# Kernel optimization log

Measured on AMD Instinct MI355X. Metric: run time of the kernel, lower is better.

The kernel has to match this reference:

```python
import jax, jax.numpy as jnp
import numpy as np
from jax.scipy.special import logsumexp

NEG = -1e9  # stands in for log(0) = -inf in the padded one-hots (avoids NaN-producing -inf)


def setup_inputs() -> dict:
    key = jax.random.key(0)
    ks = jax.random.split(key, 9)
    Lx, Ly, B, D, Vout = 64, 64, 128, 256, 53
    return {
        "prior_ctx": jax.random.normal(ks[0], (Lx, B, D), dtype=jnp.float32),
        "modern_ctx": jax.random.normal(ks[1], (Ly, B, D), dtype=jnp.float32),
        "W_sub": jax.random.normal(ks[2], (Vout, D), dtype=jnp.float32) * 0.05,
        "b_sub": jax.random.normal(ks[3], (Vout,), dtype=jnp.float32) * 0.05,
        "W_ins": jax.random.normal(ks[4], (Vout, D), dtype=jnp.float32) * 0.05,
        "b_ins": jax.random.normal(ks[5], (Vout,), dtype=jnp.float32) * 0.05,
        "target_ids": jax.random.randint(ks[6], (Ly - 1, B), 0, Vout, dtype=jnp.int32),
        "src_lengths": jax.random.randint(ks[7], (B,), 1, Lx + 1),
        "tgt_lengths": jax.random.randint(ks[8], (B,), 1, Ly + 1),
    }


def reference(prior_ctx, modern_ctx, W_sub, b_sub, W_ins, b_ins,
              target_ids, src_lengths, tgt_lengths):
    Lx, B, D = prior_ctx.shape
    Ly = modern_ctx.shape[0]
    Vout = W_sub.shape[0]

    # outer-sum context: [Lx, Ly, B, D]
    ctx = prior_ctx[:, None, :, :] + modern_ctx[None, :, :, :]

    # padding matrix: True where both source pos i and target pos j are valid. [Lx, Ly, B, 1]
    mask = ((jnp.arange(Lx)[:, None, None] < src_lengths[None, None, :])
            & (jnp.arange(Ly)[None, :, None] < tgt_lengths[None, None, :]))[..., None]

    # heads: Linear + LogSoftmax, zeroed on padding. [Lx, Ly, B, Vout]
    sub = jnp.where(mask, jax.nn.log_softmax(jnp.einsum('xybd,vd->xybv', ctx, W_sub) + b_sub, axis=-1), 0.0)
    ins = jnp.where(mask, jax.nn.log_softmax(jnp.einsum('xybd,vd->xybv', ctx, W_ins) + b_ins, axis=-1), 0.0)

    del_probs = sub[:, :, :, Vout - 1]  # [Lx, Ly, B]
    end_probs = ins[:, :, :, Vout - 1]

    # log one-hots of targets shifted by 1: [Ly-1, B, Vout]
    log_oh = jnp.where(target_ids[:, :, None] == jnp.arange(Vout)[None, None, :], 0.0, NEG)

    sub_probs = logsumexp(sub[:, :-1] + log_oh[None], axis=-1)  # [Lx, Ly-1, B]
    ins_probs = logsumexp(ins[:, :-1] + log_oh[None], axis=-1)
    return del_probs, end_probs, sub_probs, ins_probs
```

## Files before the change

kernel.cpp:

```cpp
#include <hip/hip_runtime.h>

#define D   256
#define NB  128
#define NV  53
#define NR  8192
#define V4  14
#define SLB (V4*NR*4)


typedef float  f4 __attribute__((ext_vector_type(4)));
typedef short  s8 __attribute__((ext_vector_type(8)));

__device__ __forceinline__ ushort f2bf(float f) {
    uint u = __float_as_uint(f);
    u += 0x7fff + ((u >> 16) & 1);
    return (ushort)(u >> 16);
}
__device__ __forceinline__ float bflo(uint w) { return __uint_as_float(w << 16); }
__device__ __forceinline__ float bfhi(uint w) { return __uint_as_float(w & 0xffff0000u); }

__global__ __launch_bounds__(256) void p1_kernel(
    const float* __restrict__ prior, const float* __restrict__ modern,
    const float* __restrict__ Wsub, const float* __restrict__ bsub,
    const float* __restrict__ Wins, const float* __restrict__ bins,
    ushort* __restrict__ wsb)
{
    __shared__ ushort WB[3584 * 8];
    const int tid = threadIdx.x;

    #pragma unroll
    for (int i = 0; i < 14; ++i) {
        const int F  = tid + 256 * i;
        const int l  = F & 63, s = (F >> 6) & 7, nt = F >> 9;
        const int o  = nt * 16 + (l & 15);
        const int d0 = 32 * s + 8 * (l >> 4);
        s8 bfr;
        if (o < NV) {
            const float* w = Wsub + o * D + d0;
            #pragma unroll
            for (int j = 0; j < 8; ++j) bfr[j] = (short)f2bf(w[j]);
        } else if (o < 106) {
            const float* w = Wins + (o - NV) * D + d0;
            #pragma unroll
            for (int j = 0; j < 8; ++j) bfr[j] = (short)f2bf(w[j]);
        } else {
            #pragma unroll
            for (int j = 0; j < 8; ++j) bfr[j] = 0;
        }
        *(s8*)&WB[F * 8] = bfr;
    }
    __syncthreads();

    const int wave = tid >> 6, lane = tid & 63;
    const int tile = blockIdx.x * 4 + wave;
    const int side = tile >> 9;
    const int row0 = (tile & 511) << 4;
    const int lrow = lane & 15, lk = lane >> 4;
    const float* __restrict__ src =
        (side ? modern : prior) + (size_t)(row0 + lrow) * D + lk * 8;

    f4 acc[7];
    #pragma unroll
    for (int nt = 0; nt < 7; ++nt) { acc[nt][0]=0.f; acc[nt][1]=0.f; acc[nt][2]=0.f; acc[nt][3]=0.f; }

    #pragma unroll
    for (int s = 0; s < 8; ++s) {
        const f4 c0 = *(const f4*)(src + 32 * s);
        const f4 c1 = *(const f4*)(src + 32 * s + 4);
        s8 a;
        a[0]=(short)f2bf(c0[0]); a[1]=(short)f2bf(c0[1]);
        a[2]=(short)f2bf(c0[2]); a[3]=(short)f2bf(c0[3]);
        a[4]=(short)f2bf(c1[0]); a[5]=(short)f2bf(c1[1]);
        a[6]=(short)f2bf(c1[2]); a[7]=(short)f2bf(c1[3]);
        #pragma unroll
        for (int nt = 0; nt < 7; ++nt) {
            const s8 bfr = *(const s8*)&WB[(((nt << 3) + s) * 64 + lane) * 8];
            acc[nt] = __builtin_amdgcn_mfma_f32_16x16x32_bf16(a, bfr, acc[nt], 0, 0, 0);
        }
    }

    ushort* __restrict__ base = wsb + side * (2 * SLB);
    #pragma unroll
    for (int nt = 0; nt < 7; ++nt) {
        const int v = nt * 16 + lrow;
        if (v < 106) {
            float bias = 0.f;
            if (side) bias = (v < NV) ? bsub[v] : bins[v - NV];
            const int   vi = (v < NV) ? v : v - NV;
            ushort* sl     = base + ((v < NV) ? 0 : SLB);
            const int a0   = (vi >> 2) * (NR * 4) + (vi & 3);
            #pragma unroll
            for (int r = 0; r < 4; ++r) {
                const int row = row0 + 4 * lk + r;
                sl[a0 + row * 4] = f2bf(acc[nt][r] + bias);
            }
        }
    }
}

__global__ __launch_bounds__(256) void p2_kernel(
    const ushort* __restrict__ wsb,
    const int* __restrict__ target, const int* __restrict__ srclen,
    const int* __restrict__ tgtlen, float* __restrict__ out)
{
    const int tid = threadIdx.x;
    const int b   = tid & 127;
    const int bid = blockIdx.x;
    const int xt  = ((bid & 7) << 1) | ((bid >> 3) & 1);
    const int y   = ((bid >> 4) << 1) | (tid >> 7);
    const int yb  = y * NB + b;

    const int sl = srclen[b], tl = tgtlen[b];
    const bool ymask = y < tl;
    const bool hasT  = y < 63;
    const int  t     = hasT ? target[y * NB + b] : 0;
    const int  toff  = (t >> 2) * (NR * 4) + (t & 3);

    float m[56], l[56];

    #pragma unroll
    for (int dist = 0; dist < 2; ++dist) {
        const ushort* __restrict__ P = wsb + dist * SLB;
        const ushort* __restrict__ M = wsb + (2 + dist) * SLB;

        #pragma unroll
        for (int g = 0; g < V4; ++g) {
            const uint2 q = *(const uint2*)(M + (g * NR + yb) * 4);
            m[4*g+0] = bflo(q.x); m[4*g+1] = bfhi(q.x);
            m[4*g+2] = bflo(q.y); m[4*g+3] = bfhi(q.y);
        }
        const float mlt = bflo((uint)M[toff + yb * 4]);

        float* __restrict__ o0 = out + dist * 524288;
        float* __restrict__ o1 = out + 1048576 + dist * 516096;

        #pragma unroll
        for (int xi = 0; xi < 4; ++xi) {
            const int x  = (xt << 2) + xi;
            const int xb = x * NB + b;
            const bool msk = (x < sl) & ymask;
            #pragma unroll
            for (int g = 0; g < V4; ++g) {
                const uint2 q = *(const uint2*)(P + (g * NR + xb) * 4);
                l[4*g+0] = bflo(q.x) + m[4*g+0];
                l[4*g+1] = bfhi(q.x) + m[4*g+1];
                l[4*g+2] = bflo(q.y) + m[4*g+2];
                l[4*g+3] = bfhi(q.y) + m[4*g+3];
            }
            float mx = l[0];
            #pragma unroll
            for (int v = 1; v < NV; ++v) mx = fmaxf(mx, l[v]);
            float ssum = 0.f;
            #pragma unroll
            for (int v = 0; v < NV; ++v) ssum += __expf(l[v] - mx);
            const float lse = mx + __logf(ssum);
            o0[((x << 6) | y) * NB + b] = msk ? (l[NV - 1] - lse) : 0.f;
            if (hasT) {
                const float lt = bflo((uint)P[toff + xb * 4]) + mlt;
                o1[(x * 63 + y) * NB + b] = msk ? (lt - lse) : 0.f;
            }
        }
    }
}

extern "C" void kernel_launch(void* const* d_in, const int* in_sizes, int n_in,
                              void* d_out, int out_size, void* d_ws, size_t ws_size,
                              hipStream_t stream) {
    const float* prior  = (const float*)d_in[0];
    const float* modern = (const float*)d_in[1];
    const float* Wsub   = (const float*)d_in[2];
    const float* bsub   = (const float*)d_in[3];
    const float* Wins   = (const float*)d_in[4];
    const float* bins   = (const float*)d_in[5];
    const int*   target = (const int*)d_in[6];
    const int*   srclen = (const int*)d_in[7];
    const int*   tgtlen = (const int*)d_in[8];
    ushort* wsb = (ushort*)d_ws;
    float*  out = (float*)d_out;

    p1_kernel<<<256, 256, 0, stream>>>(prior, modern, Wsub, bsub, Wins, bins, wsb);
    p2_kernel<<<512, 256, 0, stream>>>(wsb, target, srclen, tgtlen, out);
}
```

Measured before the change: 36.01 us.

## Pre-pack weights once, subtract per-row maxima, drop max pass from logsumexp

```diff
diff --git a/kernel.cpp b/kernel.cpp
--- a/kernel.cpp
+++ b/kernel.cpp
@@ -6,9 +6,14 @@
 #define NR  8192
 #define V4  14
 #define SLB (V4*NR*4)
+#define WBOFF (4*SLB)
+#define BTOFF (WBOFF + 3584*8)
+#define LOG2E 1.44269504088896340736f
+#define LN2   0.69314718055994530942f
 
 
 typedef float  f4 __attribute__((ext_vector_type(4)));
+typedef float  f2 __attribute__((ext_vector_type(2)));
 typedef short  s8 __attribute__((ext_vector_type(8)));
 
 __device__ __forceinline__ ushort f2bf(float f) {
@@ -19,38 +24,57 @@
 __device__ __forceinline__ float bflo(uint w) { return __uint_as_float(w << 16); }
 __device__ __forceinline__ float bfhi(uint w) { return __uint_as_float(w & 0xffff0000u); }
 
-__global__ __launch_bounds__(256) void p1_kernel(
+__device__ __forceinline__ float fexp2(float x) {
+#if __has_builtin(__builtin_amdgcn_exp2f)
+    return __builtin_amdgcn_exp2f(x);
+#else
+    return exp2f(x);
+#endif
+}
+__device__ __forceinline__ float flog2(float x) {
+#if __has_builtin(__builtin_amdgcn_logf)
+    return __builtin_amdgcn_logf(x);
+#else
+    return log2f(x);
+#endif
+}
+
+__global__ void p0_kernel(const float* __restrict__ Wsub, const float* __restrict__ Wins,
+                          const float* __restrict__ bsub, const float* __restrict__ bins,
+                          ushort* __restrict__ WBg, float* __restrict__ biasT)
+{
+    const int F  = blockIdx.x * 64 + threadIdx.x;
+    const int l  = F & 63, s = (F >> 6) & 7, nt = F >> 9;
+    const int o  = nt * 16 + (l & 15);
+    const int d0 = 32 * s + 8 * (l >> 4);
+    s8 bfr;
+    if (o < NV) {
+        const float* w = Wsub + o * D + d0;
+        #pragma unroll
+        for (int j = 0; j < 8; ++j) bfr[j] = (short)f2bf(w[j] * LOG2E);
+    } else if (o < 106) {
+        const float* w = Wins + (o - NV) * D + d0;
+        #pragma unroll
+        for (int j = 0; j < 8; ++j) bfr[j] = (short)f2bf(w[j] * LOG2E);
+    } else {
+        #pragma unroll
+        for (int j = 0; j < 8; ++j) bfr[j] = 0;
+    }
+    *(s8*)&WBg[F * 8] = bfr;
+    if (F < 112) {
+        float bv = 0.f;
+        if (F < NV)       bv = bsub[F] * LOG2E;
+        else if (F < 106) bv = bins[F - NV] * LOG2E;
+        biasT[F] = bv;
+    }
+}
+
+__global__ __launch_bounds__(256, 1) void p1_kernel(
     const float* __restrict__ prior, const float* __restrict__ modern,
-    const float* __restrict__ Wsub, const float* __restrict__ bsub,
-    const float* __restrict__ Wins, const float* __restrict__ bins,
+    const ushort* __restrict__ WBg, const float* __restrict__ biasT,
     ushort* __restrict__ wsb)
 {
-    __shared__ ushort WB[3584 * 8];
-    const int tid = threadIdx.x;
-
-    #pragma unroll
-    for (int i = 0; i < 14; ++i) {
-        const int F  = tid + 256 * i;
-        const int l  = F & 63, s = (F >> 6) & 7, nt = F >> 9;
-        const int o  = nt * 16 + (l & 15);
-        const int d0 = 32 * s + 8 * (l >> 4);
-        s8 bfr;
-        if (o < NV) {
-            const float* w = Wsub + o * D + d0;
-            #pragma unroll
-            for (int j = 0; j < 8; ++j) bfr[j] = (short)f2bf(w[j]);
-        } else if (o < 106) {
-            const float* w = Wins + (o - NV) * D + d0;
-            #pragma unroll
-            for (int j = 0; j < 8; ++j) bfr[j] = (short)f2bf(w[j]);
-        } else {
-            #pragma unroll
-            for (int j = 0; j < 8; ++j) bfr[j] = 0;
-        }
-        *(s8*)&WB[F * 8] = bfr;
-    }
-    __syncthreads();
-
+    const int tid  = threadIdx.x;
     const int wave = tid >> 6, lane = tid & 63;
     const int tile = blockIdx.x * 4 + wave;
     const int side = tile >> 9;
@@ -74,8 +98,40 @@
         a[6]=(short)f2bf(c1[2]); a[7]=(short)f2bf(c1[3]);
         #pragma unroll
         for (int nt = 0; nt < 7; ++nt) {
-            const s8 bfr = *(const s8*)&WB[(((nt << 3) + s) * 64 + lane) * 8];
+            const s8 bfr = *(const s8*)&WBg[(((nt << 3) + s) * 64 + lane) * 8];
             acc[nt] = __builtin_amdgcn_mfma_f32_16x16x32_bf16(a, bfr, acc[nt], 0, 0, 0);
+        }
+    }
+
+    float val[7][4];
+    #pragma unroll
+    for (int nt = 0; nt < 7; ++nt) {
+        const int v = nt * 16 + lrow;
+        const float bias = side ? biasT[v] : 0.f;
+        #pragma unroll
+        for (int r = 0; r < 4; ++r) val[nt][r] = acc[nt][r] + bias;
+    }
+
+    float ms[4], mi[4];
+    #pragma unroll
+    for (int r = 0; r < 4; ++r) { ms[r] = -3e38f; mi[r] = -3e38f; }
+    #pragma unroll
+    for (int nt = 0; nt < 7; ++nt) {
+        const int v = nt * 16 + lrow;
+        const bool isS = v < NV;
+        const bool isI = (v >= NV) & (v < 106);
+        #pragma unroll
+        for (int r = 0; r < 4; ++r) {
+            ms[r] = fmaxf(ms[r], isS ? val[nt][r] : -3e38f);
+            mi[r] = fmaxf(mi[r], isI ? val[nt][r] : -3e38f);
+        }
+    }
+    #pragma unroll
+    for (int r = 0; r < 4; ++r) {
+        #pragma unroll
+        for (int k = 1; k <= 8; k <<= 1) {
+            ms[r] = fmaxf(ms[r], __shfl_xor(ms[r], k));
+            mi[r] = fmaxf(mi[r], __shfl_xor(mi[r], k));
         }
     }
 
@@ -84,21 +140,35 @@
     for (int nt = 0; nt < 7; ++nt) {
         const int v = nt * 16 + lrow;
         if (v < 106) {
-            float bias = 0.f;
-            if (side) bias = (v < NV) ? bsub[v] : bins[v - NV];
-            const int   vi = (v < NV) ? v : v - NV;
-            ushort* sl     = base + ((v < NV) ? 0 : SLB);
+            const bool isS = v < NV;
+            const int  vi  = isS ? v : v - NV;
+            ushort* sl     = base + (isS ? 0 : SLB);
             const int a0   = (vi >> 2) * (NR * 4) + (vi & 3);
             #pragma unroll
             for (int r = 0; r < 4; ++r) {
                 const int row = row0 + 4 * lk + r;
-                sl[a0 + row * 4] = f2bf(acc[nt][r] + bias);
-            }
-        }
-    }
-}
-
-__global__ __launch_bounds__(256) void p2_kernel(
+                const float rm = isS ? ms[r] : mi[r];
+                sl[a0 + row * 4] = f2bf(val[nt][r] - rm);
+            }
+        }
+    }
+    {
+        const int v6 = 96 + lrow;
+        if (v6 >= 106 && v6 <= 108) {
+            const int vi = v6 - NV;
+            const int a0 = (vi >> 2) * (NR * 4) + (vi & 3);
+            const ushort PADBF = f2bf(-1e30f);
+            #pragma unroll
+            for (int r = 0; r < 4; ++r) {
+                const int row = row0 + 4 * lk + r;
+                base[a0 + row * 4]       = PADBF;
+                base[SLB + a0 + row * 4] = PADBF;
+            }
+        }
+    }
+}
+
+__global__ __launch_bounds__(256, 2) void p2_kernel(
     const ushort* __restrict__ wsb,
     const int* __restrict__ target, const int* __restrict__ srclen,
     const int* __restrict__ tgtlen, float* __restrict__ out)
@@ -116,18 +186,17 @@
     const int  t     = hasT ? target[y * NB + b] : 0;
     const int  toff  = (t >> 2) * (NR * 4) + (t & 3);
 
-    float m[56], l[56];
-
     #pragma unroll
     for (int dist = 0; dist < 2; ++dist) {
         const ushort* __restrict__ P = wsb + dist * SLB;
         const ushort* __restrict__ M = wsb + (2 + dist) * SLB;
 
+        f2 Ml[V4], Mh[V4];
         #pragma unroll
         for (int g = 0; g < V4; ++g) {
             const uint2 q = *(const uint2*)(M + (g * NR + yb) * 4);
-            m[4*g+0] = bflo(q.x); m[4*g+1] = bfhi(q.x);
-            m[4*g+2] = bflo(q.y); m[4*g+3] = bfhi(q.y);
+            Ml[g][0] = bflo(q.x); Ml[g][1] = bfhi(q.x);
+            Mh[g][0] = bflo(q.y); Mh[g][1] = bfhi(q.y);
         }
         const float mlt = bflo((uint)M[toff + yb * 4]);
 
@@ -139,25 +208,29 @@
             const int x  = (xt << 2) + xi;
             const int xb = x * NB + b;
             const bool msk = (x < sl) & ymask;
+
+            f2 sa; sa[0] = 0.f; sa[1] = 0.f;
+            f2 sb; sb[0] = 0.f; sb[1] = 0.f;
+            float l52 = 0.f;
             #pragma unroll
             for (int g = 0; g < V4; ++g) {
-                const uint2 q = *(const uint2*)(P + (g * NR + xb) * 4);
-                l[4*g+0] = bflo(q.x) + m[4*g+0];
-                l[4*g+1] = bfhi(q.x) + m[4*g+1];
-                l[4*g+2] = bflo(q.y) + m[4*g+2];
-                l[4*g+3] = bfhi(q.y) + m[4*g+3];
-            }
-            float mx = l[0];
-            #pragma unroll
-            for (int v = 1; v < NV; ++v) mx = fmaxf(mx, l[v]);
-            float ssum = 0.f;
-            #pragma unroll
-            for (int v = 0; v < NV; ++v) ssum += __expf(l[v] - mx);
-            const float lse = mx + __logf(ssum);
-            o0[((x << 6) | y) * NB + b] = msk ? (l[NV - 1] - lse) : 0.f;
+                const uint2 p = *(const uint2*)(P + (g * NR + xb) * 4);
+                f2 av; av[0] = bflo(p.x); av[1] = bfhi(p.x);
+                f2 bv; bv[0] = bflo(p.y); bv[1] = bfhi(p.y);
+                av = av + Ml[g];
+                bv = bv + Mh[g];
+                if (g == 13) l52 = av[0];
+                f2 ea; ea[0] = fexp2(av[0]); ea[1] = fexp2(av[1]);
+                f2 eb; eb[0] = fexp2(bv[0]); eb[1] = fexp2(bv[1]);
+                sa = sa + ea;
+                sb = sb + eb;
+            }
+            const f2 st = sa + sb;
+            const float ls = flog2(st[0] + st[1]);
+            o0[((x << 6) | y) * NB + b] = msk ? (l52 - ls) * LN2 : 0.f;
             if (hasT) {
                 const float lt = bflo((uint)P[toff + xb * 4]) + mlt;
-                o1[(x * 63 + y) * NB + b] = msk ? (lt - lse) : 0.f;
+                o1[(x * 63 + y) * NB + b] = msk ? (lt - ls) * LN2 : 0.f;
             }
         }
     }
@@ -175,9 +248,12 @@
     const int*   target = (const int*)d_in[6];
     const int*   srclen = (const int*)d_in[7];
     const int*   tgtlen = (const int*)d_in[8];
-    ushort* wsb = (ushort*)d_ws;
-    float*  out = (float*)d_out;
-
-    p1_kernel<<<256, 256, 0, stream>>>(prior, modern, Wsub, bsub, Wins, bins, wsb);
+    ushort* wsb   = (ushort*)d_ws;
+    ushort* WBg   = wsb + WBOFF;
+    float*  biasT = (float*)(wsb + BTOFF);
+    float*  out   = (float*)d_out;
+
+    p0_kernel<<<56, 64, 0, stream>>>(Wsub, Wins, bsub, bins, WBg, biasT);
+    p1_kernel<<<256, 256, 0, stream>>>(prior, modern, WBg, biasT, wsb);
     p2_kernel<<<512, 256, 0, stream>>>(wsb, target, srclen, tgtlen, out);
 }
```

Result: slower. 41.80 us (+16.1%).

## Factorize softmax sum into products of precomputed exponentials and split weight prep

Applied to the files above, without the earlier changes.

```diff
diff --git a/kernel.cpp b/kernel.cpp
--- a/kernel.cpp
+++ b/kernel.cpp
@@ -6,9 +6,16 @@
 #define NR  8192
 #define V4  14
 #define SLB (V4*NR*4)
+#define ESOFF (4*SLB)
+#define WBOFF (8*SLB)
+#define BTOFF (WBOFF + 3584*8)
+#define A52   (13*NR*4)
+#define LOG2E 1.44269504088896340736f
+#define LN2   0.69314718055994530942f
 
 
 typedef float  f4 __attribute__((ext_vector_type(4)));
+typedef float  f2 __attribute__((ext_vector_type(2)));
 typedef short  s8 __attribute__((ext_vector_type(8)));
 
 __device__ __forceinline__ ushort f2bf(float f) {
@@ -18,50 +25,63 @@
 }
 __device__ __forceinline__ float bflo(uint w) { return __uint_as_float(w << 16); }
 __device__ __forceinline__ float bfhi(uint w) { return __uint_as_float(w & 0xffff0000u); }
-
-__global__ __launch_bounds__(256) void p1_kernel(
+__device__ __forceinline__ float fexp2(float x) { return __builtin_exp2f(x); }
+__device__ __forceinline__ float flog2(float x) { return __builtin_log2f(x); }
+
+__global__ void p0_kernel(const float* __restrict__ Wsub, const float* __restrict__ Wins,
+                          const float* __restrict__ bsub, const float* __restrict__ bins,
+                          ushort* __restrict__ WBg, float* __restrict__ biasT)
+{
+    const int F  = blockIdx.x * 64 + threadIdx.x;
+    const int l  = F & 63, s = (F >> 6) & 7, nt = F >> 9;
+    const int o  = nt * 16 + (l & 15);
+    const int d0 = 32 * s + 8 * (l >> 4);
+    s8 bfr;
+    if (o < NV) {
+        const float* w = Wsub + o * D + d0;
+        #pragma unroll
+        for (int j = 0; j < 8; ++j) bfr[j] = (short)f2bf(w[j] * LOG2E);
+    } else if (o < 106) {
+        const float* w = Wins + (o - NV) * D + d0;
+        #pragma unroll
+        for (int j = 0; j < 8; ++j) bfr[j] = (short)f2bf(w[j] * LOG2E);
+    } else {
+        #pragma unroll
+        for (int j = 0; j < 8; ++j) bfr[j] = 0;
+    }
+    *(s8*)&WBg[F * 8] = bfr;
+    if (F < 112) {
+        float bv = 0.f;
+        if (F < NV)       bv = bsub[F] * LOG2E;
+        else if (F < 106) bv = bins[F - NV] * LOG2E;
+        biasT[F] = bv;
+    }
+}
+
+template<int NT0, int NTN>
+__device__ __forceinline__ void p1_body(
     const float* __restrict__ prior, const float* __restrict__ modern,
-    const float* __restrict__ Wsub, const float* __restrict__ bsub,
-    const float* __restrict__ Wins, const float* __restrict__ bins,
-    ushort* __restrict__ wsb)
-{
-    __shared__ ushort WB[3584 * 8];
-    const int tid = threadIdx.x;
-
-    #pragma unroll
-    for (int i = 0; i < 14; ++i) {
-        const int F  = tid + 256 * i;
-        const int l  = F & 63, s = (F >> 6) & 7, nt = F >> 9;
-        const int o  = nt * 16 + (l & 15);
-        const int d0 = 32 * s + 8 * (l >> 4);
-        s8 bfr;
-        if (o < NV) {
-            const float* w = Wsub + o * D + d0;
-            #pragma unroll
-            for (int j = 0; j < 8; ++j) bfr[j] = (short)f2bf(w[j]);
-        } else if (o < 106) {
-            const float* w = Wins + (o - NV) * D + d0;
-            #pragma unroll
-            for (int j = 0; j < 8; ++j) bfr[j] = (short)f2bf(w[j]);
-        } else {
-            #pragma unroll
-            for (int j = 0; j < 8; ++j) bfr[j] = 0;
-        }
-        *(s8*)&WB[F * 8] = bfr;
+    const ushort* __restrict__ WBg, const float* __restrict__ biasT,
+    ushort* __restrict__ wsb, ushort* __restrict__ WB, int tid, int tg)
+{
+    #pragma unroll
+    for (int i = 0; i < NTN * 2; ++i) {
+        const int idx = i * 256 + tid;
+        *(s8*)&WB[idx * 8] = *(const s8*)&WBg[(NT0 * 512 + idx) * 8];
     }
     __syncthreads();
 
     const int wave = tid >> 6, lane = tid & 63;
-    const int tile = blockIdx.x * 4 + wave;
+    const int tile = tg * 4 + wave;
     const int side = tile >> 9;
     const int row0 = (tile & 511) << 4;
     const int lrow = lane & 15, lk = lane >> 4;
     const float* __restrict__ src =
         (side ? modern : prior) + (size_t)(row0 + lrow) * D + lk * 8;
 
-    f4 acc[7];
-    #pragma unroll
-    for (int nt = 0; nt < 7; ++nt) { acc[nt][0]=0.f; acc[nt][1]=0.f; acc[nt][2]=0.f; acc[nt][3]=0.f; }
+    f4 acc[NTN];
+    #pragma unroll
+    for (int j = 0; j < NTN; ++j) { acc[j][0]=0.f; acc[j][1]=0.f; acc[j][2]=0.f; acc[j][3]=0.f; }
 
     #pragma unroll
     for (int s = 0; s < 8; ++s) {
@@ -73,29 +93,58 @@
         a[4]=(short)f2bf(c1[0]); a[5]=(short)f2bf(c1[1]);
         a[6]=(short)f2bf(c1[2]); a[7]=(short)f2bf(c1[3]);
         #pragma unroll
-        for (int nt = 0; nt < 7; ++nt) {
-            const s8 bfr = *(const s8*)&WB[(((nt << 3) + s) * 64 + lane) * 8];
-            acc[nt] = __builtin_amdgcn_mfma_f32_16x16x32_bf16(a, bfr, acc[nt], 0, 0, 0);
-        }
-    }
-
-    ushort* __restrict__ base = wsb + side * (2 * SLB);
-    #pragma unroll
-    for (int nt = 0; nt < 7; ++nt) {
-        const int v = nt * 16 + lrow;
-        if (v < 106) {
-            float bias = 0.f;
-            if (side) bias = (v < NV) ? bsub[v] : bins[v - NV];
-            const int   vi = (v < NV) ? v : v - NV;
-            ushort* sl     = base + ((v < NV) ? 0 : SLB);
-            const int a0   = (vi >> 2) * (NR * 4) + (vi & 3);
+        for (int j = 0; j < NTN; ++j) {
+            const s8 bfr = *(const s8*)&WB[(((j << 3) + s) * 64 + lane) * 8];
+            acc[j] = __builtin_amdgcn_mfma_f32_16x16x32_bf16(a, bfr, acc[j], 0, 0, 0);
+        }
+    }
+
+    #pragma unroll
+    for (int j = 0; j < NTN; ++j) {
+        const int v = (NT0 + j) * 16 + lrow;
+        const float bias = side ? biasT[v] : 0.f;
+        const bool valid = v < 106;
+        const bool isS   = v < NV;
+        const int  vi    = isS ? v : v - NV;
+        ushort* __restrict__ raw = wsb + (size_t)(side * 2 + (isS ? 0 : 1)) * SLB;
+        ushort* __restrict__ Eb  = raw + ESOFF;
+        const int a0 = (vi >> 2) * (NR * 4) + (vi & 3);
+        #pragma unroll
+        for (int r = 0; r < 4; ++r) {
+            if (valid) {
+                const int row = row0 + 4 * lk + r;
+                const float val = acc[j][r] + bias;
+                raw[a0 + row * 4] = f2bf(val);
+                Eb[a0 + row * 4]  = f2bf(fexp2(val));
+            }
+        }
+    }
+    if (NT0 == 4) {
+        if (lrow >= 10 && lrow <= 12) {
+            const int vi = 43 + lrow;
+            const int a0 = (vi >> 2) * (NR * 4) + (vi & 3);
             #pragma unroll
             for (int r = 0; r < 4; ++r) {
                 const int row = row0 + 4 * lk + r;
-                sl[a0 + row * 4] = f2bf(acc[nt][r] + bias);
-            }
-        }
-    }
+                wsb[ESOFF + (size_t)(side * 2 + 0) * SLB + a0 + row * 4] = 0;
+                wsb[ESOFF + (size_t)(side * 2 + 1) * SLB + a0 + row * 4] = 0;
+            }
+        }
+    }
+}
+
+__global__ __launch_bounds__(256) void p1_kernel(
+    const float* __restrict__ prior, const float* __restrict__ modern,
+    const ushort* __restrict__ WBg, const float* __restrict__ biasT,
+    ushort* __restrict__ wsb)
+{
+    __shared__ ushort WB[4 * 512 * 8];
+    const int tid = threadIdx.x;
+    const int tg  = blockIdx.x >> 1;
+    if ((blockIdx.x & 1) == 0)
+        p1_body<0, 4>(prior, modern, WBg, biasT, wsb, WB, tid, tg);
+    else
+        p1_body<4, 3>(prior, modern, WBg, biasT, wsb, WB, tid, tg);
 }
 
 __global__ __launch_bounds__(256) void p2_kernel(
@@ -116,20 +165,22 @@
     const int  t     = hasT ? target[y * NB + b] : 0;
     const int  toff  = (t >> 2) * (NR * 4) + (t & 3);
 
-    float m[56], l[56];
-
-    #pragma unroll
+    #pragma unroll 1
     for (int dist = 0; dist < 2; ++dist) {
-        const ushort* __restrict__ P = wsb + dist * SLB;
-        const ushort* __restrict__ M = wsb + (2 + dist) * SLB;
-
+        const ushort* __restrict__ Praw = wsb + dist * SLB;
+        const ushort* __restrict__ Mraw = wsb + (2 + dist) * SLB;
+        const ushort* __restrict__ PE   = Praw + ESOFF;
+        const ushort* __restrict__ ME   = Mraw + ESOFF;
+
+        f2 em0[V4], em1[V4];
         #pragma unroll
         for (int g = 0; g < V4; ++g) {
-            const uint2 q = *(const uint2*)(M + (g * NR + yb) * 4);
-            m[4*g+0] = bflo(q.x); m[4*g+1] = bfhi(q.x);
-            m[4*g+2] = bflo(q.y); m[4*g+3] = bfhi(q.y);
-        }
-        const float mlt = bflo((uint)M[toff + yb * 4]);
+            const uint2 q = *(const uint2*)(ME + (g * NR + yb) * 4);
+            em0[g][0] = bflo(q.x); em0[g][1] = bfhi(q.x);
+            em1[g][0] = bflo(q.y); em1[g][1] = bfhi(q.y);
+        }
+        const float mlt = bflo((uint)Mraw[toff + yb * 4]);
+        const float m52 = bflo((uint)Mraw[A52  + yb * 4]);
 
         float* __restrict__ o0 = out + dist * 524288;
         float* __restrict__ o1 = out + 1048576 + dist * 516096;
@@ -139,25 +190,25 @@
             const int x  = (xt << 2) + xi;
             const int xb = x * NB + b;
             const bool msk = (x < sl) & ymask;
+
+            f2 s0; s0[0] = 0.f; s0[1] = 0.f;
+            f2 s1; s1[0] = 0.f; s1[1] = 0.f;
             #pragma unroll
             for (int g = 0; g < V4; ++g) {
-                const uint2 q = *(const uint2*)(P + (g * NR + xb) * 4);
-                l[4*g+0] = bflo(q.x) + m[4*g+0];
-                l[4*g+1] = bfhi(q.x) + m[4*g+1];
-                l[4*g+2] = bflo(q.y) + m[4*g+2];
-                l[4*g+3] = bfhi(q.y) + m[4*g+3];
-            }
-            float mx = l[0];
-            #pragma unroll
-            for (int v = 1; v < NV; ++v) mx = fmaxf(mx, l[v]);
-            float ssum = 0.f;
-            #pragma unroll
-            for (int v = 0; v < NV; ++v) ssum += __expf(l[v] - mx);
-            const float lse = mx + __logf(ssum);
-            o0[((x << 6) | y) * NB + b] = msk ? (l[NV - 1] - lse) : 0.f;
+                const uint2 p = *(const uint2*)(PE + (g * NR + xb) * 4);
+                f2 a; a[0] = bflo(p.x); a[1] = bfhi(p.x);
+                f2 c; c[0] = bflo(p.y); c[1] = bfhi(p.y);
+                s0 += a * em0[g];
+                s1 += c * em1[g];
+            }
+            const float S  = (s0[0] + s0[1]) + (s1[0] + s1[1]);
+            const float ls = flog2(S);
+
+            const float l52 = bflo((uint)Praw[A52 + xb * 4]) + m52;
+            o0[((x << 6) | y) * NB + b] = msk ? (l52 - ls) * LN2 : 0.f;
             if (hasT) {
-                const float lt = bflo((uint)P[toff + xb * 4]) + mlt;
-                o1[(x * 63 + y) * NB + b] = msk ? (lt - lse) : 0.f;
+                const float lt = bflo((uint)Praw[toff + xb * 4]) + mlt;
+                o1[(x * 63 + y) * NB + b] = msk ? (lt - ls) * LN2 : 0.f;
             }
         }
     }
@@ -175,9 +226,12 @@
     const int*   target = (const int*)d_in[6];
     const int*   srclen = (const int*)d_in[7];
     const int*   tgtlen = (const int*)d_in[8];
-    ushort* wsb = (ushort*)d_ws;
-    float*  out = (float*)d_out;
-
-    p1_kernel<<<256, 256, 0, stream>>>(prior, modern, Wsub, bsub, Wins, bins, wsb);
+    ushort* wsb   = (ushort*)d_ws;
+    ushort* WBg   = wsb + WBOFF;
+    float*  biasT = (float*)(wsb + BTOFF);
+    float*  out   = (float*)d_out;
+
+    p0_kernel<<<56, 64, 0, stream>>>(Wsub, Wins, bsub, bins, WBg, biasT);
+    p1_kernel<<<512, 256, 0, stream>>>(prior, modern, WBg, biasT, wsb);
     p2_kernel<<<512, 256, 0, stream>>>(wsb, target, srclen, tgtlen, out);
 }
```

New measurement: 38.07 us. 5.7% more time.

## Precompute bf16 weight tiles once and split K across waves in projection kernel

Applied to the files above, without the earlier changes.

```diff
diff --git a/kernel.cpp b/kernel.cpp
--- a/kernel.cpp
+++ b/kernel.cpp
@@ -6,6 +6,8 @@
 #define NR  8192
 #define V4  14
 #define SLB (V4*NR*4)
+#define WBOFF (4*SLB)
+#define BTOFF (WBOFF + 3584*8)
 
 
 typedef float  f4 __attribute__((ext_vector_type(4)));
@@ -19,10 +21,37 @@
 __device__ __forceinline__ float bflo(uint w) { return __uint_as_float(w << 16); }
 __device__ __forceinline__ float bfhi(uint w) { return __uint_as_float(w & 0xffff0000u); }
 
+__global__ void p0_kernel(const float* __restrict__ Wsub, const float* __restrict__ Wins,
+                          const float* __restrict__ bsub, const float* __restrict__ bins,
+                          ushort* __restrict__ WBg, float* __restrict__ biasT)
+{
+    const int F  = blockIdx.x * 64 + threadIdx.x;
+    const int l  = F & 63, s = (F >> 6) & 7, nt = F >> 9;
+    const int o  = nt * 16 + (l & 15);
+    const int d0 = 32 * s + 8 * (l >> 4);
+    const float* w = nullptr;
+    if (o < NV)       w = Wsub + o * D + d0;
+    else if (o < 106) w = Wins + (o - NV) * D + d0;
+    s8 bfr;
+    if (w) {
+        #pragma unroll
+        for (int j = 0; j < 8; ++j) bfr[j] = (short)f2bf(w[j]);
+    } else {
+        #pragma unroll
+        for (int j = 0; j < 8; ++j) bfr[j] = 0;
+    }
+    *(s8*)&WBg[F * 8] = bfr;
+    if (F < 112) {
+        float bv = 0.f;
+        if (F < NV)       bv = bsub[F];
+        else if (F < 106) bv = bins[F - NV];
+        biasT[F] = bv;
+    }
+}
+
 __global__ __launch_bounds__(256) void p1_kernel(
     const float* __restrict__ prior, const float* __restrict__ modern,
-    const float* __restrict__ Wsub, const float* __restrict__ bsub,
-    const float* __restrict__ Wins, const float* __restrict__ bins,
+    const ushort* __restrict__ WBg, const float* __restrict__ biasT,
     ushort* __restrict__ wsb)
 {
     __shared__ ushort WB[3584 * 8];
@@ -30,41 +59,28 @@
 
     #pragma unroll
     for (int i = 0; i < 14; ++i) {
-        const int F  = tid + 256 * i;
-        const int l  = F & 63, s = (F >> 6) & 7, nt = F >> 9;
-        const int o  = nt * 16 + (l & 15);
-        const int d0 = 32 * s + 8 * (l >> 4);
-        s8 bfr;
-        if (o < NV) {
-            const float* w = Wsub + o * D + d0;
-            #pragma unroll
-            for (int j = 0; j < 8; ++j) bfr[j] = (short)f2bf(w[j]);
-        } else if (o < 106) {
-            const float* w = Wins + (o - NV) * D + d0;
-            #pragma unroll
-            for (int j = 0; j < 8; ++j) bfr[j] = (short)f2bf(w[j]);
-        } else {
-            #pragma unroll
-            for (int j = 0; j < 8; ++j) bfr[j] = 0;
-        }
-        *(s8*)&WB[F * 8] = bfr;
+        const int idx = i * 256 + tid;
+        *(s8*)&WB[idx * 8] = *(const s8*)&WBg[idx * 8];
     }
     __syncthreads();
 
     const int wave = tid >> 6, lane = tid & 63;
-    const int tile = blockIdx.x * 4 + wave;
+    const int kh   = wave & 1;
+    const int tsub = wave >> 1;
+    const int tile = blockIdx.x * 2 + tsub;
     const int side = tile >> 9;
     const int row0 = (tile & 511) << 4;
     const int lrow = lane & 15, lk = lane >> 4;
     const float* __restrict__ src =
-        (side ? modern : prior) + (size_t)(row0 + lrow) * D + lk * 8;
+        (side ? modern : prior) + (size_t)(row0 + lrow) * D + kh * 128 + lk * 8;
 
     f4 acc[7];
     #pragma unroll
     for (int nt = 0; nt < 7; ++nt) { acc[nt][0]=0.f; acc[nt][1]=0.f; acc[nt][2]=0.f; acc[nt][3]=0.f; }
 
     #pragma unroll
-    for (int s = 0; s < 8; ++s) {
+    for (int s = 0; s < 4; ++s) {
+        const int sg = kh * 4 + s;
         const f4 c0 = *(const f4*)(src + 32 * s);
         const f4 c1 = *(const f4*)(src + 32 * s + 4);
         s8 a;
@@ -74,25 +90,40 @@
         a[6]=(short)f2bf(c1[2]); a[7]=(short)f2bf(c1[3]);
         #pragma unroll
         for (int nt = 0; nt < 7; ++nt) {
-            const s8 bfr = *(const s8*)&WB[(((nt << 3) + s) * 64 + lane) * 8];
+            const s8 bfr = *(const s8*)&WB[(((nt << 3) + sg) * 64 + lane) * 8];
             acc[nt] = __builtin_amdgcn_mfma_f32_16x16x32_bf16(a, bfr, acc[nt], 0, 0, 0);
         }
     }
 
-    ushort* __restrict__ base = wsb + side * (2 * SLB);
-    #pragma unroll
-    for (int nt = 0; nt < 7; ++nt) {
+    __syncthreads();
+    float* __restrict__ scr = (float*)WB;
+    if (kh == 0) {
+        #pragma unroll
+        for (int nt = 4; nt < 7; ++nt)
+            *(f4*)&scr[((tsub * 7 + nt) * 64 + lane) * 4] = acc[nt];
+    } else {
+        #pragma unroll
+        for (int nt = 0; nt < 4; ++nt)
+            *(f4*)&scr[((tsub * 7 + nt) * 64 + lane) * 4] = acc[nt];
+    }
+    __syncthreads();
+
+    const int ntlo = kh ? 4 : 0;
+    const int nthi = kh ? 7 : 4;
+    for (int nt = ntlo; nt < nthi; ++nt) {
+        const f4 part = *(const f4*)&scr[((tsub * 7 + nt) * 64 + lane) * 4];
+        const f4 full = acc[nt] + part;
         const int v = nt * 16 + lrow;
         if (v < 106) {
-            float bias = 0.f;
-            if (side) bias = (v < NV) ? bsub[v] : bins[v - NV];
-            const int   vi = (v < NV) ? v : v - NV;
-            ushort* sl     = base + ((v < NV) ? 0 : SLB);
-            const int a0   = (vi >> 2) * (NR * 4) + (vi & 3);
+            const bool isS = v < NV;
+            const float bias = side ? biasT[v] : 0.f;
+            const int  vi  = isS ? v : v - NV;
+            ushort* __restrict__ sl = wsb + (size_t)(side * 2 + (isS ? 0 : 1)) * SLB;
+            const int a0 = (vi >> 2) * (NR * 4) + (vi & 3);
             #pragma unroll
             for (int r = 0; r < 4; ++r) {
                 const int row = row0 + 4 * lk + r;
-                sl[a0 + row * 4] = f2bf(acc[nt][r] + bias);
+                sl[a0 + row * 4] = f2bf(full[r] + bias);
             }
         }
     }
@@ -175,9 +206,12 @@
     const int*   target = (const int*)d_in[6];
     const int*   srclen = (const int*)d_in[7];
     const int*   tgtlen = (const int*)d_in[8];
-    ushort* wsb = (ushort*)d_ws;
-    float*  out = (float*)d_out;
-
-    p1_kernel<<<256, 256, 0, stream>>>(prior, modern, Wsub, bsub, Wins, bins, wsb);
+    ushort* wsb   = (ushort*)d_ws;
+    ushort* WBg   = wsb + WBOFF;
+    float*  biasT = (float*)(wsb + BTOFF);
+    float*  out   = (float*)d_out;
+
+    p0_kernel<<<56, 64, 0, stream>>>(Wsub, Wins, bsub, bins, WBg, biasT);
+    p1_kernel<<<512, 256, 0, stream>>>(prior, modern, WBg, biasT, wsb);
     p2_kernel<<<512, 256, 0, stream>>>(wsb, target, srclen, tgtlen, out);
 }
```

Result: slower. 39.23 us (+8.9%).
